# Performance work log

Hardware: AMD Instinct MI355X
Metric: run time of the kernel (lower is better)

The kernel has to match this reference:

```python
import jax, jax.numpy as jnp
import numpy as np

B, N, K = 4, 4096, 16
DP, DM = 128, 256  # d_points, d_model


def setup_inputs() -> dict:
    key = jax.random.key(0)
    ks = jax.random.split(key, 10)
    w = lambda k, s: (jax.random.normal(k, s) * 0.02).astype(jnp.float32)
    return dict(
        features=jax.random.normal(ks[0], (B, N, DP), dtype=jnp.float32),
        xyz=jax.random.normal(ks[1], (B, N, 3), dtype=jnp.float32),
        fc1_w=w(ks[2], (DP, DM)), fc1_b=jnp.zeros((DM,), jnp.float32),
        fc2_w=w(ks[3], (DM, DP)), fc2_b=jnp.zeros((DP,), jnp.float32),
        fd1_w=w(ks[4], (3, DM)), fd1_b=jnp.zeros((DM,), jnp.float32),
        fd2_w=w(ks[5], (DM, DM)), fd2_b=jnp.zeros((DM,), jnp.float32),
        wq=w(ks[6], (DM, DM)), wk=w(ks[7], (DM, DM)), wv=w(ks[8], (DM, DM)),
    )


def reference(features, xyz, fc1_w, fc1_b, fc2_w, fc2_b,
              fd1_w, fd1_b, fd2_w, fd2_b, wq, wk, wv):
    # KNN of xyz against itself (includes self, distance-sorted ascending)
    sq = jnp.sum(xyz * xyz, axis=-1)                                 # [B,N]
    d2 = sq[:, :, None] + sq[:, None, :] - 2.0 * jnp.einsum('bnc,bmc->bnm', xyz, xyz)
    _, knn_idx = jax.lax.top_k(-d2, K)                               # [B,N,K]
    gather = jax.vmap(lambda pts, idx: pts[idx])                     # [B,N,C],[B,N,K]->[B,N,K,C]
    knn_xyz = gather(xyz, knn_idx)                                   # [B,N,K,3]

    x = features @ fc1_w + fc1_b                                     # [B,N,DM]
    q = x @ wq                                                       # [B,N,DM]
    kf = gather(x @ wk, knn_idx)                                     # [B,N,K,DM]
    vf = gather(x @ wv, knn_idx)                                     # [B,N,K,DM]

    delta = xyz[:, :, None, :] - knn_xyz                             # [B,N,K,3]
    pos = jax.nn.relu(delta @ fd1_w + fd1_b) @ fd2_w + fd2_b         # [B,N,K,DM]

    logits = jnp.einsum('bnd,bnkd->bnk', q, kf + pos) / np.sqrt(DM).astype(np.float32)
    attn = jax.nn.softmax(logits, axis=-1)                           # [B,N,K]
    res = jnp.einsum('bnk,bnkd->bnd', attn, vf + pos)                # [B,N,DM]

    out = res @ fc2_w + fc2_b + features                             # [B,N,DP]
    return jnp.transpose(out, (0, 2, 1))                             # [B,DP,N]
```

## Files before the change

### kernel.cpp

```cpp
#include <hip/hip_runtime.h>
#include <hip/hip_bf16.h>
#include <hip/hip_fp16.h>
#include <math.h>

#define B_   4
#define N_   4096
#define K_   16
#define DP_  128
#define DM_  256
#define NPTS (B_ * N_)
#define SEG_ 16
#define CAND_ (N_ / SEG_)
#define QPAD 136

typedef unsigned int u32;
typedef unsigned char u8;
typedef _Float16 f16;
typedef __attribute__((ext_vector_type(2))) __fp16 h2;
typedef __attribute__((ext_vector_type(8))) _Float16 f16x8;
typedef __attribute__((ext_vector_type(4))) float floatx4;

static __device__ __forceinline__ h2 pkrtz(float a, float b) {
    return __builtin_amdgcn_cvt_pkrtz(a, b);
}
static __device__ __forceinline__ u32 asu32(h2 h) { return __builtin_bit_cast(u32, h); }
static __device__ __forceinline__ h2 ash2(u32 u) { return __builtin_bit_cast(h2, u); }

#define CEXA(x, y) { u32 _lo = min(x, y); y = max(x, y); x = _lo; }
#define CEXD(x, y) { u32 _hi = max(x, y); y = min(x, y); x = _hi; }

static __device__ __forceinline__ void sort16_desc(u32 c[16]) {
    CEXD(c[0],c[1]);  CEXD(c[2],c[3]);  CEXD(c[4],c[5]);  CEXD(c[6],c[7]);
    CEXD(c[8],c[9]);  CEXD(c[10],c[11]); CEXD(c[12],c[13]); CEXD(c[14],c[15]);
    CEXD(c[0],c[2]);  CEXD(c[1],c[3]);  CEXD(c[4],c[6]);  CEXD(c[5],c[7]);
    CEXD(c[8],c[10]); CEXD(c[9],c[11]); CEXD(c[12],c[14]); CEXD(c[13],c[15]);
    CEXD(c[1],c[2]);  CEXD(c[5],c[6]);  CEXD(c[9],c[10]); CEXD(c[13],c[14]);
    CEXD(c[0],c[4]);  CEXD(c[1],c[5]);  CEXD(c[2],c[6]);  CEXD(c[3],c[7]);
    CEXD(c[8],c[12]); CEXD(c[9],c[13]); CEXD(c[10],c[14]); CEXD(c[11],c[15]);
    CEXD(c[2],c[4]);  CEXD(c[3],c[5]);  CEXD(c[10],c[12]); CEXD(c[11],c[13]);
    CEXD(c[1],c[2]);  CEXD(c[3],c[4]);  CEXD(c[5],c[6]);
    CEXD(c[9],c[10]); CEXD(c[11],c[12]); CEXD(c[13],c[14]);
    CEXD(c[0],c[8]);  CEXD(c[1],c[9]);  CEXD(c[2],c[10]); CEXD(c[3],c[11]);
    CEXD(c[4],c[12]); CEXD(c[5],c[13]); CEXD(c[6],c[14]); CEXD(c[7],c[15]);
    CEXD(c[4],c[8]);  CEXD(c[5],c[9]);  CEXD(c[6],c[10]); CEXD(c[7],c[11]);
    CEXD(c[2],c[4]);  CEXD(c[3],c[5]);  CEXD(c[6],c[8]);  CEXD(c[7],c[9]);
    CEXD(c[10],c[12]); CEXD(c[11],c[13]);
    CEXD(c[1],c[2]);  CEXD(c[3],c[4]);  CEXD(c[5],c[6]);  CEXD(c[7],c[8]);
    CEXD(c[9],c[10]); CEXD(c[11],c[12]); CEXD(c[13],c[14]);
}

static __device__ __forceinline__ void remerge16_asc(u32 L[16]) {
    CEXA(L[0],L[8]);  CEXA(L[1],L[9]);  CEXA(L[2],L[10]); CEXA(L[3],L[11]);
    CEXA(L[4],L[12]); CEXA(L[5],L[13]); CEXA(L[6],L[14]); CEXA(L[7],L[15]);
    CEXA(L[0],L[4]);  CEXA(L[1],L[5]);  CEXA(L[2],L[6]);  CEXA(L[3],L[7]);
    CEXA(L[8],L[12]); CEXA(L[9],L[13]); CEXA(L[10],L[14]); CEXA(L[11],L[15]);
    CEXA(L[0],L[2]);  CEXA(L[1],L[3]);  CEXA(L[4],L[6]);  CEXA(L[5],L[7]);
    CEXA(L[8],L[10]); CEXA(L[9],L[11]); CEXA(L[12],L[14]); CEXA(L[13],L[15]);
    CEXA(L[0],L[1]);  CEXA(L[2],L[3]);  CEXA(L[4],L[5]);  CEXA(L[6],L[7]);
    CEXA(L[8],L[9]);  CEXA(L[10],L[11]); CEXA(L[12],L[13]); CEXA(L[14],L[15]);
}

static __device__ void knn_part_body(float4* sc, const float* __restrict__ xyz,
                                     u32* __restrict__ part, int id)
{
    const int xblk = id & 15;
    const int s = (id >> 4) & 15;
    const int b = id >> 8;
    const int n = xblk * 256 + threadIdx.x;
    const float* xb = xyz + (size_t)b * N_ * 3;
    const float x0 = xb[n * 3 + 0], x1 = xb[n * 3 + 1], x2 = xb[n * 3 + 2];
    const float nx0 = -x0, nx1 = -x1, nx2 = -x2;
    const float hs = 0.5f * fmaf(x0, x0, fmaf(x1, x1, x2 * x2));
    const u32 kmask = 0xFFFFF000u;

    {
        const int m = s * CAND_ + threadIdx.x;
        const float a0 = xb[m * 3 + 0];
        const float a1 = xb[m * 3 + 1];
        const float a2 = xb[m * 3 + 2];
        sc[threadIdx.x] = make_float4(a0, a1, a2, 0.5f * (a0 * a0 + a1 * a1 + a2 * a2));
    }
    __syncthreads();

    u32 L[16];
#pragma unroll
    for (int i = 0; i < 16; ++i) L[i] = 0xFFFFFFFFu;

    const u32 ibase = (u32)(s * CAND_);
    for (int m0 = 0; m0 < CAND_; m0 += 16) {
        float4 cc[16];
#pragma unroll
        for (int t = 0; t < 16; ++t) cc[t] = sc[m0 + t];
        u32 c[16];
#pragma unroll
        for (int t = 0; t < 16; ++t) {
            const float e = fmaf(nx0, cc[t].x,
                            fmaf(nx1, cc[t].y,
                            fmaf(nx2, cc[t].z, cc[t].w + hs)));
            c[t] = (__float_as_uint(fmaxf(e, 0.0f)) & kmask) | (ibase + (u32)(m0 + t));
        }
        sort16_desc(c);
#pragma unroll
        for (int i = 0; i < 16; ++i) L[i] = min(L[i], c[i]);
        remerge16_asc(L);
    }

    const int p = b * N_ + n;
#pragma unroll
    for (int j = 0; j < 16; ++j)
        part[(size_t)(s * 16 + j) * NPTS + p] = L[j];
}

static __device__ void prep_body(float (*t)[33],
    const float* __restrict__ wq, const float* __restrict__ wk, const float* __restrict__ wv,
    const float* __restrict__ fd2, const float* __restrict__ fc1, const float* __restrict__ fc2,
    const float* __restrict__ feat,
    f16* __restrict__ catW, f16* __restrict__ fc2T, f16* __restrict__ bt2,
    f16* __restrict__ fd2c, f16* __restrict__ wqc, f16* __restrict__ fc1c,
    f16* __restrict__ featb, int bx, int by, int job)
{
    const int tid = threadIdx.x;

    if (job < 4) {
        const float* in; int R, C;
        switch (job) {
            case 0: in = wq;  R = DM_; C = DM_; break;
            case 1: in = wk;  R = DM_; C = DM_; break;
            case 2: in = wv;  R = DM_; C = DM_; break;
            default: in = fc2; R = DM_; C = DP_; break;
        }
        const int c0 = bx * 32, r0 = by * 32;
        if (c0 >= C || r0 >= R) return;
        const int lx = tid & 31, ly = tid >> 5;
#pragma unroll
        for (int i = 0; i < 32; i += 8)
            t[ly + i][lx] = in[(size_t)(r0 + ly + i) * C + c0 + lx];
        __syncthreads();
#pragma unroll
        for (int i = 0; i < 32; i += 8) {
            const int c = c0 + ly + i;
            const f16 v = (f16)t[lx][ly + i];
            int n;
            switch (job) {
                case 0: n = c; break;
                case 1: n = 256 + ((c >> 2) << 3) + (c & 3); break;
                case 2: n = 256 + ((c >> 2) << 3) + 4 + (c & 3); break;
                default: n = -1; break;
            }
            if (job < 3) {
                catW[(size_t)n * DM_ + r0 + lx] = v;
            } else {
                fc2T[(size_t)c * DM_ + r0 + lx] = v;
                bt2[(size_t)c * 512 + 256 + r0 + lx] = v;
            }
        }
    } else {
        const int bid = by * 8 + bx;
        const int tId = bid * 256 + tid;
        const float* in; f16* outp; int n4;
        if (job == 4)      { in = fd2;  outp = fd2c;  n4 = (DM_ * DM_) / 4; }
        else if (job == 5) { in = wq;   outp = wqc;   n4 = (DM_ * DM_) / 4; }
        else if (job == 6) { in = fc1;  outp = fc1c;  n4 = (DP_ * DM_) / 4; }
        else               { in = feat; outp = featb; n4 = (NPTS * DP_) / 4; }
        for (int i = tId; i < n4; i += 16384) {
            const float4 v = ((const float4*)in)[i];
            const u32 lo = asu32(pkrtz(v.x, v.y));
            const u32 hi = asu32(pkrtz(v.z, v.w));
            ((uint2*)outp)[i] = make_uint2(lo, hi);
        }
    }
}

__global__ __launch_bounds__(256) void fused_prep_knn_kernel(
    const float* __restrict__ wq, const float* __restrict__ wk, const float* __restrict__ wv,
    const float* __restrict__ fd2, const float* __restrict__ fc1, const float* __restrict__ fc2,
    const float* __restrict__ feat,
    f16* __restrict__ catW, f16* __restrict__ fc2T, f16* __restrict__ bt2,
    f16* __restrict__ fd2c, f16* __restrict__ wqc, f16* __restrict__ fc1c,
    f16* __restrict__ featb,
    const float* __restrict__ xyz, u32* __restrict__ part)
{
    __shared__ __align__(16) char smem[4352];
    const int id = blockIdx.x;
    if (id < 512) {
        prep_body((float(*)[33])smem, wq, wk, wv, fd2, fc1, fc2, feat,
                  catW, fc2T, bt2, fd2c, wqc, fc1c, featb,
                  id & 7, (id >> 3) & 7, id >> 6);
    } else {
        knn_part_body((float4*)smem, xyz, part, id - 512);
    }
}

static __device__ void gemm_tile(f16* As, f16* Bs,
    const f16* __restrict__ A, const f16* __restrict__ Bt,
    f16* __restrict__ Cb,
    int M, int N, int K, int ldc, int bx, int by)
{
    const int tid = threadIdx.x;
    const int m0 = by * 128, n0 = bx * 128;
    const int w = tid >> 6, l = tid & 63;
    const int wm = (w >> 1) * 64, wn = (w & 1) * 64;
    const int fm = l & 15, kq = l >> 4;

    floatx4 acc[4][4];
#pragma unroll
    for (int i = 0; i < 4; ++i)
#pragma unroll
        for (int j = 0; j < 4; ++j)
            acc[i][j] = (floatx4){0.0f, 0.0f, 0.0f, 0.0f};

    for (int k0 = 0; k0 < K; k0 += 32) {
        __syncthreads();
#pragma unroll
        for (int c = 0; c < 2; ++c) {
            const int li = tid + c * 256;
            const int row = li >> 2, part = li & 3;
            *(uint4*)&As[row * 32 + part * 8] =
                *(const uint4*)&A[(size_t)(m0 + row) * K + k0 + part * 8];
            *(uint4*)&Bs[row * 32 + part * 8] =
                *(const uint4*)&Bt[(size_t)(n0 + row) * K + k0 + part * 8];
        }
        __syncthreads();
        f16x8 af[4], bf[4];
#pragma unroll
        for (int i = 0; i < 4; ++i)
            af[i] = *(const f16x8*)&As[(wm + i * 16 + fm) * 32 + kq * 8];
#pragma unroll
        for (int j = 0; j < 4; ++j)
            bf[j] = *(const f16x8*)&Bs[(wn + j * 16 + fm) * 32 + kq * 8];
#pragma unroll
        for (int i = 0; i < 4; ++i)
#pragma unroll
            for (int j = 0; j < 4; ++j)
                acc[i][j] = __builtin_amdgcn_mfma_f32_16x16x32_f16(af[i], bf[j], acc[i][j], 0, 0, 0);
    }

#pragma unroll
    for (int i = 0; i < 4; ++i) {
#pragma unroll
        for (int j = 0; j < 4; ++j) {
            const int col = n0 + wn + j * 16 + fm;
            const int rowb = m0 + wm + i * 16 + kq * 4;
#pragma unroll
            for (int r = 0; r < 4; ++r)
                Cb[(size_t)(rowb + r) * ldc + col] = (f16)acc[i][j][r];
        }
    }
}

__global__ __launch_bounds__(256) void gemm_qkv_kernel(
    const f16* __restrict__ A,
    const f16* __restrict__ Bt,
    const float* __restrict__ bias,
    f16* __restrict__ Cb)
{
    __shared__ __align__(16) f16 As[128 * QPAD];
    __shared__ __align__(16) f16 Bs[128 * QPAD];
    const int tid = threadIdx.x;
    const int m0 = blockIdx.y * 128, n0 = blockIdx.x * 128;
    const int w = tid >> 6, l = tid & 63;
    const int wm = (w >> 1) * 64, wn = (w & 1) * 64;
    const int fm = l & 15, kq = l >> 4;

#pragma unroll
    for (int c = 0; c < 8; ++c) {
        const int li = tid + c * 256;
        const int row = li >> 4, part = li & 15;
        *(uint4*)&As[row * QPAD + part * 8] =
            *(const uint4*)&A[(size_t)(m0 + row) * 128 + part * 8];
        *(uint4*)&Bs[row * QPAD + part * 8] =
            *(const uint4*)&Bt[(size_t)(n0 + row) * 128 + part * 8];
    }
    __syncthreads();

    floatx4 acc[4][4];
#pragma unroll
    for (int i = 0; i < 4; ++i)
#pragma unroll
        for (int j = 0; j < 4; ++j)
            acc[i][j] = (floatx4){0.0f, 0.0f, 0.0f, 0.0f};

#pragma unroll
    for (int kk = 0; kk < 4; ++kk) {
        f16x8 af[4], bf[4];
#pragma unroll
        for (int i = 0; i < 4; ++i)
            af[i] = *(const f16x8*)&As[(wm + i * 16 + fm) * QPAD + kk * 32 + kq * 8];
#pragma unroll
        for (int j = 0; j < 4; ++j)
            bf[j] = *(const f16x8*)&Bs[(wn + j * 16 + fm) * QPAD + kk * 32 + kq * 8];
#pragma unroll
        for (int i = 0; i < 4; ++i)
#pragma unroll
            for (int j = 0; j < 4; ++j)
                acc[i][j] = __builtin_amdgcn_mfma_f32_16x16x32_f16(af[i], bf[j], acc[i][j], 0, 0, 0);
    }

#pragma unroll
    for (int i = 0; i < 4; ++i) {
#pragma unroll
        for (int j = 0; j < 4; ++j) {
            const int col = n0 + wn + j * 16 + fm;
            const int rowb = m0 + wm + i * 16 + kq * 4;
#pragma unroll
            for (int r = 0; r < 4; ++r)
                Cb[(size_t)(rowb + r) * 1024 + col] = (f16)(acc[i][j][r] + bias[col]);
        }
    }
}

__global__ __launch_bounds__(256) void gemm_out_kernel(
    const f16* __restrict__ A,
    const f16* __restrict__ Bt,
    const float* __restrict__ bias2,
    const float* __restrict__ feat,
    float* __restrict__ CT)
{
    __shared__ __align__(16) f16 As[64 * 32];
    __shared__ __align__(16) f16 Bs[128 * 32];
    const int tid = threadIdx.x;
    const int m0 = blockIdx.x * 64;
    const int w = tid >> 6, l = tid & 63;
    const int wn = w * 32;
    const int fm = l & 15, kq = l >> 4;

    floatx4 acc[4][2];
#pragma unroll
    for (int i = 0; i < 4; ++i)
#pragma unroll
        for (int j = 0; j < 2; ++j)
            acc[i][j] = (floatx4){0.0f, 0.0f, 0.0f, 0.0f};

    for (int k0 = 0; k0 < 512; k0 += 32) {
        __syncthreads();
        {
            const int row = tid >> 2, part = tid & 3;
            *(uint4*)&As[row * 32 + part * 8] =
                *(const uint4*)&A[(size_t)(m0 + row) * 512 + k0 + part * 8];
        }
#pragma unroll
        for (int c = 0; c < 2; ++c) {
            const int li = tid + c * 256;
            const int row = li >> 2, part = li & 3;
            *(uint4*)&Bs[row * 32 + part * 8] =
                *(const uint4*)&Bt[(size_t)row * 512 + k0 + part * 8];
        }
        __syncthreads();
        f16x8 af[4], bf[2];
#pragma unroll
        for (int i = 0; i < 4; ++i)
            af[i] = *(const f16x8*)&As[(i * 16 + fm) * 32 + kq * 8];
#pragma unroll
        for (int j = 0; j < 2; ++j)
            bf[j] = *(const f16x8*)&Bs[(wn + j * 16 + fm) * 32 + kq * 8];
#pragma unroll
        for (int i = 0; i < 4; ++i)
#pragma unroll
            for (int j = 0; j < 2; ++j)
                acc[i][j] = __builtin_amdgcn_mfma_f32_16x16x32_f16(af[i], bf[j], acc[i][j], 0, 0, 0);
    }

#pragma unroll
    for (int i = 0; i < 4; ++i) {
#pragma unroll
        for (int j = 0; j < 2; ++j) {
            const int col = wn + j * 16 + fm;
            const int rowb = m0 + i * 16 + kq * 4;
            float4 vv;
#pragma unroll
            for (int r = 0; r < 4; ++r)
                ((float*)&vv)[r] = acc[i][j][r] + bias2[col]
                                 + feat[(size_t)(rowb + r) * DP_ + col];
            const int bb = rowb >> 12;
            *(float4*)&CT[(size_t)(bb * DP_ + col) * N_ + (rowb & (N_ - 1))] = vv;
        }
    }
}

static __device__ void kvw_body(const f16* __restrict__ qkv, const float* __restrict__ xyz,
                                const float* __restrict__ fd1_w, const float* __restrict__ fd1_b,
                                u8* __restrict__ kvw, f16* __restrict__ ubuf, int id)
{
    const int t = id * 256 + threadIdx.x;
    const int p = t >> 6, g = t & 63;
    const uint4 kv = *(const uint4*)(qkv + (size_t)p * 1024 + 256 + g * 8);
    const h2 k01 = ash2(kv.x), k23 = ash2(kv.y), v01 = ash2(kv.z), v23 = ash2(kv.w);
    int lo = 0, hi = 0;
    lo = __builtin_amdgcn_cvt_pk_fp8_f32((float)k01.x, (float)k01.y, lo, false);
    lo = __builtin_amdgcn_cvt_pk_fp8_f32((float)k23.x, (float)k23.y, lo, true);
    hi = __builtin_amdgcn_cvt_pk_fp8_f32((float)v01.x, (float)v01.y, hi, false);
    hi = __builtin_amdgcn_cvt_pk_fp8_f32((float)v23.x, (float)v23.y, hi, true);

    const float x0 = xyz[(size_t)p * 3 + 0];
    const float x1 = xyz[(size_t)p * 3 + 1];
    const float x2 = xyz[(size_t)p * 3 + 2];
    const int c0 = g * 4;
    const float4 w0v = *(const float4*)&fd1_w[c0];
    const float4 w1v = *(const float4*)&fd1_w[DM_ + c0];
    const float4 w2v = *(const float4*)&fd1_w[2 * DM_ + c0];
    const float4 b1v = *(const float4*)&fd1_b[c0];
    const float ww0 = x0 * w0v.x + x1 * w1v.x + x2 * w2v.x;
    const float ww1 = x0 * w0v.y + x1 * w1v.y + x2 * w2v.y;
    const float ww2 = x0 * w0v.z + x1 * w1v.z + x2 * w2v.z;
    const float ww3 = x0 * w0v.w + x1 * w1v.w + x2 * w2v.w;

    uint4 row;
    row.x = (u32)lo;
    row.y = (u32)hi;
    row.z = asu32(pkrtz(ww0, ww1));
    row.w = asu32(pkrtz(ww2, ww3));
    *(uint4*)(kvw + (size_t)p * 1024 + g * 16) = row;

    const uint2 uu = make_uint2(asu32(pkrtz(ww0 + b1v.x, ww1 + b1v.y)),
                                asu32(pkrtz(ww2 + b1v.z, ww3 + b1v.w)));
    *(uint2*)(ubuf + (size_t)p * 256 + c0) = uu;
}

static __device__ void mergeAB_body(const u32* __restrict__ part, int* __restrict__ knn_idx,
                                    int id)
{
    const int p = id * 256 + threadIdx.x;
    const int b = p >> 12;

    u32 L[16];
#pragma unroll
    for (int i = 0; i < 16; ++i) L[i] = 0xFFFFFFFFu;

    for (int s = 0; s < SEG_; ++s) {
        u32 seg[16];
#pragma unroll
        for (int j = 0; j < 16; ++j)
            seg[j] = part[(size_t)(s * 16 + j) * NPTS + p];
#pragma unroll
        for (int i = 0; i < 16; ++i) L[i] = min(L[i], seg[15 - i]);
        remerge16_asc(L);
    }

    int* o = knn_idx + (size_t)p * K_;
#pragma unroll
    for (int i = 0; i < 16; ++i) o[i] = b * N_ + (int)(L[i] & 0xFFFu);
}

__global__ __launch_bounds__(256) void fused_kvwmerge_kernel(
    const f16* __restrict__ qkv, const float* __restrict__ xyz,
    const float* __restrict__ fd1_w, const float* __restrict__ fd1_b,
    u8* __restrict__ kvw, f16* __restrict__ ubuf,
    const u32* __restrict__ part, int* __restrict__ knn_idx)
{
    const int id = blockIdx.x;
    if (id < NPTS * 64 / 256) kvw_body(qkv, xyz, fd1_w, fd1_b, kvw, ubuf, id);
    else                      mergeAB_body(part, knn_idx, id - NPTS * 64 / 256);
}

__global__ __launch_bounds__(256) void fused_small1_kernel(
    const f16* __restrict__ fd2c, const f16* __restrict__ wqc,
    f16* __restrict__ catWqp,
    const f16* __restrict__ fc2T, f16* __restrict__ bt2)
{
    __shared__ __align__(16) f16 As[128 * 32];
    __shared__ __align__(16) f16 Bs[128 * 32];
    const int id = blockIdx.x;
    if (id < 4)
        gemm_tile(As, Bs, fd2c, wqc, catWqp, DM_, DM_, DM_, DM_, id & 1, id >> 1);
    else
        gemm_tile(As, Bs, fc2T, fd2c, bt2, DP_, DM_, DM_, 512, id - 4, 0);
}

__global__ __launch_bounds__(256) void fused_small2_kernel(
    const f16* __restrict__ catW, const f16* __restrict__ fc1c, f16* __restrict__ WallT,
    const float* __restrict__ fc1_b, const float* __restrict__ fd2_b,
    const float* __restrict__ fc2_w, const float* __restrict__ fc2_b,
    float* __restrict__ b_all, float* __restrict__ bias2)
{
    __shared__ __align__(16) f16 As[128 * 32];
    __shared__ __align__(16) f16 Bs[128 * 32];
    const int id = blockIdx.x;
    const int tid = threadIdx.x;
    if (id < 8) {
        gemm_tile(As, Bs, catW, fc1c, WallT, 1024, DP_, DM_, DP_, 0, id);
    } else if (id < 12) {
        const int n = (id - 8) * 256 + tid;
        float s = 0.0f;
        for (int j = 0; j < DM_; ++j)
            s += fc1_b[j] * (float)catW[(size_t)n * DM_ + j];
        b_all[n] = s;
    } else if (tid < DP_) {
        float s = fc2_b[tid];
        for (int t = 0; t < DM_; ++t)
            s += fd2_b[t] * fc2_w[(size_t)t * DP_ + tid];
        bias2[tid] = s;
    }
}

__global__ __launch_bounds__(256, 1) void attn_kernel(
    const f16* __restrict__ qkv, const u8* __restrict__ kvw,
    const f16* __restrict__ ubuf, const int* __restrict__ knn_idx,
    const float* __restrict__ fd2_b,
    f16* __restrict__ ab)
{
    const int wave = threadIdx.x >> 6, l = threadIdx.x & 63;
    const int bi = blockIdx.x;
    const int p = ((bi & 3) << 12) + ((bi >> 2) << 2) + wave;
    const int c0 = l * 4;

    int gi = 0;
    if (l < 16) gi = knn_idx[p * K_ + l];

    uint4 kvr[16];
#pragma unroll
    for (int k = 0; k < 16; ++k) {
        const int gik = __shfl(gi, k);
        kvr[k] = *(const uint4*)(kvw + (size_t)gik * 1024 + l * 16);
    }
    asm volatile("" ::: "memory");

    const uint2 qu  = *(const uint2*)(qkv + (size_t)p * 1024 + c0);
    const uint2 qpu = *(const uint2*)(qkv + (size_t)p * 1024 + 768 + c0);
    const uint2 uu  = *(const uint2*)(ubuf + (size_t)p * 256 + c0);
    const h2 qh01 = ash2(qu.x), qh23 = ash2(qu.y);
    const h2 qp01 = ash2(qpu.x), qp23 = ash2(qpu.y);
    const h2 u01 = ash2(uu.x), u23 = ash2(uu.y);
    const float q0 = (float)qh01.x, q1 = (float)qh01.y, q2 = (float)qh23.x, q3 = (float)qh23.y;
    const h2 zero2 = (h2)(__fp16)0.0f;

    const float4 f2b = *(const float4*)&fd2_b[c0];

    float qb;
    {
        float tq = q0 * f2b.x + q1 * f2b.y + q2 * f2b.z + q3 * f2b.w;
#pragma unroll
        for (int off = 1; off < 64; off <<= 1) tq += __shfl_xor(tq, off);
        qb = tq;
    }

    float lg[16];
    u32 h01r[16], h23r[16];
#pragma unroll
    for (int k = 0; k < 16; ++k) {
        const uint4 r = kvr[k];
        h2 d01 = u01 - ash2(r.z);
        h2 d23 = u23 - ash2(r.w);
        d01 = __builtin_elementwise_max(d01, zero2);
        d23 = __builtin_elementwise_max(d23, zero2);
        h01r[k] = asu32(d01); h23r[k] = asu32(d23);
        const auto k01 = __builtin_amdgcn_cvt_pk_f32_fp8((int)r.x, false);
        const auto k23 = __builtin_amdgcn_cvt_pk_f32_fp8((int)r.x, true);
        float t = q0 * k01[0] + q1 * k01[1] + q2 * k23[0] + q3 * k23[1];
        t = __builtin_amdgcn_fdot2(d01, qp01, t, false);
        t = __builtin_amdgcn_fdot2(d23, qp23, t, false);
#pragma unroll
        for (int off = 1; off < 64; off <<= 1) t += __shfl_xor(t, off);
        lg[k] = t;
    }

    float att[16];
    {
        float mx = -3.0e38f;
#pragma unroll
        for (int k = 0; k < 16; ++k) {
            att[k] = (lg[k] + qb) * (1.0f / 16.0f);
            mx = fmaxf(mx, att[k]);
        }
        float s = 0.0f;
#pragma unroll
        for (int k = 0; k < 16; ++k) { att[k] = __expf(att[k] - mx); s += att[k]; }
        const float inv = 1.0f / s;
#pragma unroll
        for (int k = 0; k < 16; ++k) att[k] *= inv;
    }

    float rb[4] = {0, 0, 0, 0}, hb[4] = {0, 0, 0, 0};
#pragma unroll
    for (int k = 0; k < 16; ++k) {
        const auto v01 = __builtin_amdgcn_cvt_pk_f32_fp8((int)kvr[k].y, false);
        const auto v23 = __builtin_amdgcn_cvt_pk_f32_fp8((int)kvr[k].y, true);
        const h2 hh01 = ash2(h01r[k]), hh23 = ash2(h23r[k]);
        const float a = att[k];
        rb[0] = fmaf(a, v01[0], rb[0]);
        rb[1] = fmaf(a, v01[1], rb[1]);
        rb[2] = fmaf(a, v23[0], rb[2]);
        rb[3] = fmaf(a, v23[1], rb[3]);
        hb[0] = fmaf(a, (float)hh01.x, hb[0]);
        hb[1] = fmaf(a, (float)hh01.y, hb[1]);
        hb[2] = fmaf(a, (float)hh23.x, hb[2]);
        hb[3] = fmaf(a, (float)hh23.y, hb[3]);
    }

    const uint2 ho = make_uint2(asu32(pkrtz(hb[0], hb[1])), asu32(pkrtz(hb[2], hb[3])));
    const uint2 ro = make_uint2(asu32(pkrtz(rb[0], rb[1])), asu32(pkrtz(rb[2], rb[3])));
    *(uint2*)(ab + (size_t)p * 512 + c0) = ho;
    *(uint2*)(ab + (size_t)p * 512 + 256 + c0) = ro;
}

extern "C" void kernel_launch(void* const* d_in, const int* in_sizes, int n_in,
                              void* d_out, int out_size, void* d_ws, size_t ws_size,
                              hipStream_t stream)
{
    const float* features = (const float*)d_in[0];
    const float* xyz   = (const float*)d_in[1];
    const float* fc1_w = (const float*)d_in[2];
    const float* fc1_b = (const float*)d_in[3];
    const float* fc2_w = (const float*)d_in[4];
    const float* fc2_b = (const float*)d_in[5];
    const float* fd1_w = (const float*)d_in[6];
    const float* fd1_b = (const float*)d_in[7];
    const float* fd2_w = (const float*)d_in[8];
    const float* fd2_b = (const float*)d_in[9];
    const float* wq    = (const float*)d_in[10];
    const float* wk    = (const float*)d_in[11];
    const float* wv    = (const float*)d_in[12];
    float* out = (float*)d_out;

    char* base = (char*)d_ws;
    const size_t MB = 1024 * 1024;
    u32*  part = (u32*)(base + 0);
    f16*  ab   = (f16*)(base + 0);
    u8*   kvw  = (u8*)(base + 20 * MB);
    f16*  qkv  = (f16*)(base + 36 * MB);
    f16*  featb = (f16*)(base + 68 * MB);
    int*  idx  = (int*)(base + 72 * MB);
    char* wb = base + 73 * MB;
    f16* catW  = (f16*)(wb + 0);
    f16* WallT = (f16*)(wb + 512 * 1024);
    f16* bt2   = (f16*)(wb + 768 * 1024);
    f16* fd2c  = (f16*)(wb + 896 * 1024);
    f16* wqc   = (f16*)(wb + 1024 * 1024);
    f16* fc1c  = (f16*)(wb + 1152 * 1024);
    f16* fc2T  = (f16*)(wb + 1216 * 1024);
    float* b_all = (float*)(wb + 1280 * 1024);
    float* bias2 = (float*)(wb + 1284 * 1024);
    f16*  ubuf = (f16*)(base + 76 * MB);

    const dim3 blk(256);

    fused_prep_knn_kernel<<<dim3(512 + 1024), blk, 0, stream>>>(
        wq, wk, wv, fd2_w, fc1_w, fc2_w, features,
        catW, fc2T, bt2, fd2c, wqc, fc1c, featb, xyz, part);
    fused_small1_kernel<<<dim3(6), blk, 0, stream>>>(fd2c, wqc, catW + 768 * 256, fc2T, bt2);
    fused_small2_kernel<<<dim3(13), blk, 0, stream>>>(catW, fc1c, WallT,
                                                      fc1_b, fd2_b, fc2_w, fc2_b, b_all, bias2);
    gemm_qkv_kernel<<<dim3(1024 / 128, NPTS / 128), blk, 0, stream>>>(featb, WallT, b_all, qkv);
    fused_kvwmerge_kernel<<<dim3(NPTS * 64 / 256 + NPTS / 256), blk, 0, stream>>>(
        qkv, xyz, fd1_w, fd1_b, kvw, ubuf, part, idx);
    attn_kernel<<<dim3(NPTS / 4), blk, 0, stream>>>(qkv, kvw, ubuf, idx, fd2_b, ab);
    gemm_out_kernel<<<dim3(NPTS / 64), blk, 0, stream>>>(ab, bt2, bias2, features, out);

    (void)in_sizes; (void)n_in; (void)out_size; (void)ws_size;
}
```

Measured before the change: 211.9 us.

## Split KNN candidate scan across thread pairs with packed FMA and SoA layout

Each query point is now handled by two lanes that each scan half of the 256-candidate segment, so the KNN part of the fused kernel launches twice as many blocks. The two partial top-16 lists are then merged with a cross-lane shuffle and a bitonic remerge. Candidate coordinates move to a structure-of-arrays shared-memory layout so each lane can read float4 vectors, and distances are computed with packed two-wide FMAs. This is meant to raise parallelism and cut per-lane sort work, at the cost of an extra merge step and shuffle traffic.

Measured after the change: 223.3 us. 1.05x slower.

```diff
diff --git a/kernel.cpp b/kernel.cpp
--- a/kernel.cpp
+++ b/kernel.cpp
@@ -19,6 +19,7 @@
 typedef __attribute__((ext_vector_type(2))) __fp16 h2;
 typedef __attribute__((ext_vector_type(8))) _Float16 f16x8;
 typedef __attribute__((ext_vector_type(4))) float floatx4;
+typedef __attribute__((ext_vector_type(2))) float f32x2;
 
 static __device__ __forceinline__ h2 pkrtz(float a, float b) {
     return __builtin_amdgcn_cvt_pkrtz(a, b);
@@ -60,25 +61,34 @@
     CEXA(L[8],L[9]);  CEXA(L[10],L[11]); CEXA(L[12],L[13]); CEXA(L[14],L[15]);
 }
 
-static __device__ void knn_part_body(float4* sc, const float* __restrict__ xyz,
+static __device__ void knn_part_body(float* sm, const float* __restrict__ xyz,
                                      u32* __restrict__ part, int id)
 {
-    const int xblk = id & 15;
-    const int s = (id >> 4) & 15;
-    const int b = id >> 8;
-    const int n = xblk * 256 + threadIdx.x;
+    const int xblk = id & 31;
+    const int s = (id >> 5) & 15;
+    const int b = id >> 9;
+    const int h = threadIdx.x & 1;
+    const int pi = threadIdx.x >> 1;
+    const int n = xblk * 128 + pi;
     const float* xb = xyz + (size_t)b * N_ * 3;
     const float x0 = xb[n * 3 + 0], x1 = xb[n * 3 + 1], x2 = xb[n * 3 + 2];
-    const float nx0 = -x0, nx1 = -x1, nx2 = -x2;
     const float hs = 0.5f * fmaf(x0, x0, fmaf(x1, x1, x2 * x2));
+    const f32x2 nx0 = {-x0, -x0}, nx1 = {-x1, -x1}, nx2 = {-x2, -x2};
+    const f32x2 hs2 = {hs, hs};
+    const f32x2 z2 = {0.0f, 0.0f};
     const u32 kmask = 0xFFFFF000u;
 
+    float* a0s = sm;
+    float* a1s = sm + 256;
+    float* a2s = sm + 512;
+    float* wss = sm + 768;
     {
         const int m = s * CAND_ + threadIdx.x;
-        const float a0 = xb[m * 3 + 0];
-        const float a1 = xb[m * 3 + 1];
-        const float a2 = xb[m * 3 + 2];
-        sc[threadIdx.x] = make_float4(a0, a1, a2, 0.5f * (a0 * a0 + a1 * a1 + a2 * a2));
+        const float A0 = xb[m * 3 + 0];
+        const float A1 = xb[m * 3 + 1];
+        const float A2 = xb[m * 3 + 2];
+        a0s[threadIdx.x] = A0; a1s[threadIdx.x] = A1; a2s[threadIdx.x] = A2;
+        wss[threadIdx.x] = 0.5f * (A0 * A0 + A1 * A1 + A2 * A2);
     }
     __syncthreads();
 
@@ -86,18 +96,39 @@
 #pragma unroll
     for (int i = 0; i < 16; ++i) L[i] = 0xFFFFFFFFu;
 
-    const u32 ibase = (u32)(s * CAND_);
-    for (int m0 = 0; m0 < CAND_; m0 += 16) {
-        float4 cc[16];
-#pragma unroll
-        for (int t = 0; t < 16; ++t) cc[t] = sc[m0 + t];
+    const u32 kidx = (u32)(s * CAND_ + h * 128);
+    const int qb0 = h * 32;
+    const float4* a0q = (const float4*)a0s;
+    const float4* a1q = (const float4*)a1s;
+    const float4* a2q = (const float4*)a2s;
+    const float4* wq4 = (const float4*)wss;
+
+    for (int m0 = 0; m0 < 128; m0 += 16) {
+        const int qb = qb0 + (m0 >> 2);
         u32 c[16];
 #pragma unroll
-        for (int t = 0; t < 16; ++t) {
-            const float e = fmaf(nx0, cc[t].x,
-                            fmaf(nx1, cc[t].y,
-                            fmaf(nx2, cc[t].z, cc[t].w + hs)));
-            c[t] = (__float_as_uint(fmaxf(e, 0.0f)) & kmask) | (ibase + (u32)(m0 + t));
+        for (int q = 0; q < 4; ++q) {
+            const float4 A0 = a0q[qb + q];
+            const float4 A1 = a1q[qb + q];
+            const float4 A2 = a2q[qb + q];
+            const float4 W  = wq4[qb + q];
+            f32x2 e0 = __builtin_elementwise_fma(nx0, (f32x2){A0.x, A0.y},
+                       __builtin_elementwise_fma(nx1, (f32x2){A1.x, A1.y},
+                       __builtin_elementwise_fma(nx2, (f32x2){A2.x, A2.y},
+                                                 (f32x2){W.x, W.y} + hs2)));
+            f32x2 e1 = __builtin_elementwise_fma(nx0, (f32x2){A0.z, A0.w},
+                       __builtin_elementwise_fma(nx1, (f32x2){A1.z, A1.w},
+                       __builtin_elementwise_fma(nx2, (f32x2){A2.z, A2.w},
+                                                 (f32x2){W.z, W.w} + hs2)));
+            e0 = __builtin_elementwise_max(e0, z2);
+            e1 = __builtin_elementwise_max(e1, z2);
+            const uint2 u0 = __builtin_bit_cast(uint2, e0);
+            const uint2 u1 = __builtin_bit_cast(uint2, e1);
+            const u32 kb = kidx + (u32)(m0 + q * 4);
+            c[q * 4 + 0] = (u0.x & kmask) | (kb + 0);
+            c[q * 4 + 1] = (u0.y & kmask) | (kb + 1);
+            c[q * 4 + 2] = (u1.x & kmask) | (kb + 2);
+            c[q * 4 + 3] = (u1.y & kmask) | (kb + 3);
         }
         sort16_desc(c);
 #pragma unroll
@@ -105,10 +136,17 @@
         remerge16_asc(L);
     }
 
+    u32 pl[16];
+#pragma unroll
+    for (int i = 0; i < 16; ++i) pl[i] = (u32)__shfl_xor((int)L[15 - i], 1);
+#pragma unroll
+    for (int i = 0; i < 16; ++i) L[i] = min(L[i], pl[i]);
+    remerge16_asc(L);
+
     const int p = b * N_ + n;
 #pragma unroll
-    for (int j = 0; j < 16; ++j)
-        part[(size_t)(s * 16 + j) * NPTS + p] = L[j];
+    for (int j = 0; j < 8; ++j)
+        part[(size_t)(s * 16 + h * 8 + j) * NPTS + p] = L[h * 8 + j];
 }
 
 static __device__ void prep_body(float (*t)[33],
@@ -187,7 +225,7 @@
                   catW, fc2T, bt2, fd2c, wqc, fc1c, featb,
                   id & 7, (id >> 3) & 7, id >> 6);
     } else {
-        knn_part_body((float4*)smem, xyz, part, id - 512);
+        knn_part_body((float*)smem, xyz, part, id - 512);
     }
 }
 
@@ -633,7 +671,7 @@
 
     const dim3 blk(256);
 
-    fused_prep_knn_kernel<<<dim3(512 + 1024), blk, 0, stream>>>(
+    fused_prep_knn_kernel<<<dim3(512 + 2048), blk, 0, stream>>>(
         wq, wk, wv, fd2_w, fc1_w, fc2_w, features,
         catW, fc2T, bt2, fd2c, wqc, fc1c, featb, xyz, part);
     fused_small1_kernel<<<dim3(6), blk, 0, stream>>>(fd2c, wqc, catW + 768 * 256, fc2T, bt2);
```

## Fuse QKV GEMM with KV fp8 packing and KNN merge into one kernel

Applied to the files above, without the earlier changes.

The QKV projection GEMM now has each block own 64 rows and loop over all 8 column tiles. The K/V columns are kept in shared memory and packed straight into the fp8 kvw and ubuf buffers, so the intermediate K/V never round-trips through global memory. The KNN merge blocks are appended to the same launch, which removes one kernel launch. In exchange the grid drops from 1024 GEMM blocks to 256, and about 100KB of shared memory per block limits occupancy, so parallelism and latency hiding may suffer.

Result: no change. 213.5 us (+0.8%).

```diff
diff --git a/kernel.cpp b/kernel.cpp
--- a/kernel.cpp
+++ b/kernel.cpp
@@ -248,64 +248,161 @@
     }
 }
 
-__global__ __launch_bounds__(256) void gemm_qkv_kernel(
+static __device__ void mergeAB_body(const u32* __restrict__ part, int* __restrict__ knn_idx,
+                                    int id)
+{
+    const int p = id * 256 + threadIdx.x;
+    const int b = p >> 12;
+
+    u32 L[16];
+#pragma unroll
+    for (int i = 0; i < 16; ++i) L[i] = 0xFFFFFFFFu;
+
+    for (int s = 0; s < SEG_; ++s) {
+        u32 seg[16];
+#pragma unroll
+        for (int j = 0; j < 16; ++j)
+            seg[j] = part[(size_t)(s * 16 + j) * NPTS + p];
+#pragma unroll
+        for (int i = 0; i < 16; ++i) L[i] = min(L[i], seg[15 - i]);
+        remerge16_asc(L);
+    }
+
+    int* o = knn_idx + (size_t)p * K_;
+#pragma unroll
+    for (int i = 0; i < 16; ++i) o[i] = b * N_ + (int)(L[i] & 0xFFFu);
+}
+
+#define KVP 520
+__global__ __launch_bounds__(256) void gemm_qkv_fused_kernel(
     const f16* __restrict__ A,
     const f16* __restrict__ Bt,
     const float* __restrict__ bias,
-    f16* __restrict__ Cb)
-{
-    __shared__ __align__(16) f16 As[128 * QPAD];
-    __shared__ __align__(16) f16 Bs[128 * QPAD];
+    const float* __restrict__ xyz,
+    const float* __restrict__ fd1_w, const float* __restrict__ fd1_b,
+    f16* __restrict__ Cb,
+    u8* __restrict__ kvw, f16* __restrict__ ubuf,
+    const u32* __restrict__ part, int* __restrict__ knn_idx)
+{
+    __shared__ __align__(16) f16 As[64 * 136];
+    __shared__ __align__(16) f16 Bs[128 * 136];
+    __shared__ __align__(16) f16 kvs[64 * KVP];
+    const int bid = blockIdx.x;
+    if (bid >= 256) { mergeAB_body(part, knn_idx, bid - 256); return; }
+
     const int tid = threadIdx.x;
-    const int m0 = blockIdx.y * 128, n0 = blockIdx.x * 128;
+    const int m0 = bid * 64;
     const int w = tid >> 6, l = tid & 63;
-    const int wm = (w >> 1) * 64, wn = (w & 1) * 64;
+    const int wr = (w >> 1) * 32;
+    const int wn = (w & 1) * 64;
     const int fm = l & 15, kq = l >> 4;
 
 #pragma unroll
-    for (int c = 0; c < 8; ++c) {
+    for (int c = 0; c < 4; ++c) {
         const int li = tid + c * 256;
-        const int row = li >> 4, part = li & 15;
-        *(uint4*)&As[row * QPAD + part * 8] =
-            *(const uint4*)&A[(size_t)(m0 + row) * 128 + part * 8];
-        *(uint4*)&Bs[row * QPAD + part * 8] =
-            *(const uint4*)&Bt[(size_t)(n0 + row) * 128 + part * 8];
+        const int row = li >> 4, pt = li & 15;
+        *(uint4*)&As[row * 136 + pt * 8] =
+            *(const uint4*)&A[(size_t)(m0 + row) * 128 + pt * 8];
+    }
+
+    for (int nt = 0; nt < 8; ++nt) {
+        __syncthreads();
+#pragma unroll
+        for (int c = 0; c < 8; ++c) {
+            const int li = tid + c * 256;
+            const int row = li >> 4, pt = li & 15;
+            *(uint4*)&Bs[row * 136 + pt * 8] =
+                *(const uint4*)&Bt[(size_t)(nt * 128 + row) * 128 + pt * 8];
+        }
+        __syncthreads();
+
+        floatx4 acc[2][4];
+#pragma unroll
+        for (int i = 0; i < 2; ++i)
+#pragma unroll
+            for (int j = 0; j < 4; ++j)
+                acc[i][j] = (floatx4){0.0f, 0.0f, 0.0f, 0.0f};
+
+#pragma unroll
+        for (int kk = 0; kk < 4; ++kk) {
+            f16x8 af[2], bf[4];
+#pragma unroll
+            for (int i = 0; i < 2; ++i)
+                af[i] = *(const f16x8*)&As[(wr + i * 16 + fm) * 136 + kk * 32 + kq * 8];
+#pragma unroll
+            for (int j = 0; j < 4; ++j)
+                bf[j] = *(const f16x8*)&Bs[(wn + j * 16 + fm) * 136 + kk * 32 + kq * 8];
+#pragma unroll
+            for (int i = 0; i < 2; ++i)
+#pragma unroll
+                for (int j = 0; j < 4; ++j)
+                    acc[i][j] = __builtin_amdgcn_mfma_f32_16x16x32_f16(af[i], bf[j], acc[i][j], 0, 0, 0);
+        }
+
+        if (nt >= 2 && nt < 6) {
+#pragma unroll
+            for (int i = 0; i < 2; ++i) {
+#pragma unroll
+                for (int j = 0; j < 4; ++j) {
+                    const int col = nt * 128 + wn + j * 16 + fm;
+                    const int lcol = col - 256;
+                    const int rowb = wr + i * 16 + kq * 4;
+#pragma unroll
+                    for (int r = 0; r < 4; ++r)
+                        kvs[(rowb + r) * KVP + lcol] = (f16)(acc[i][j][r] + bias[col]);
+                }
+            }
+        } else {
+#pragma unroll
+            for (int i = 0; i < 2; ++i) {
+#pragma unroll
+                for (int j = 0; j < 4; ++j) {
+                    const int col = nt * 128 + wn + j * 16 + fm;
+                    const int rowb = m0 + wr + i * 16 + kq * 4;
+#pragma unroll
+                    for (int r = 0; r < 4; ++r)
+                        Cb[(size_t)(rowb + r) * 1024 + col] = (f16)(acc[i][j][r] + bias[col]);
+                }
+            }
+        }
     }
     __syncthreads();
 
-    floatx4 acc[4][4];
-#pragma unroll
-    for (int i = 0; i < 4; ++i)
-#pragma unroll
-        for (int j = 0; j < 4; ++j)
-            acc[i][j] = (floatx4){0.0f, 0.0f, 0.0f, 0.0f};
-
-#pragma unroll
-    for (int kk = 0; kk < 4; ++kk) {
-        f16x8 af[4], bf[4];
-#pragma unroll
-        for (int i = 0; i < 4; ++i)
-            af[i] = *(const f16x8*)&As[(wm + i * 16 + fm) * QPAD + kk * 32 + kq * 8];
-#pragma unroll
-        for (int j = 0; j < 4; ++j)
-            bf[j] = *(const f16x8*)&Bs[(wn + j * 16 + fm) * QPAD + kk * 32 + kq * 8];
-#pragma unroll
-        for (int i = 0; i < 4; ++i)
-#pragma unroll
-            for (int j = 0; j < 4; ++j)
-                acc[i][j] = __builtin_amdgcn_mfma_f32_16x16x32_f16(af[i], bf[j], acc[i][j], 0, 0, 0);
-    }
-
-#pragma unroll
-    for (int i = 0; i < 4; ++i) {
-#pragma unroll
-        for (int j = 0; j < 4; ++j) {
-            const int col = n0 + wn + j * 16 + fm;
-            const int rowb = m0 + wm + i * 16 + kq * 4;
-#pragma unroll
-            for (int r = 0; r < 4; ++r)
-                Cb[(size_t)(rowb + r) * 1024 + col] = (f16)(acc[i][j][r] + bias[col]);
-        }
+    for (int it = 0; it < 16; ++it) {
+        const int task = it * 256 + tid;
+        const int pl = task >> 6, g = task & 63;
+        const int p = m0 + pl;
+        const uint4 kv = *(const uint4*)&kvs[pl * KVP + g * 8];
+        const h2 k01 = ash2(kv.x), k23 = ash2(kv.y), v01 = ash2(kv.z), v23 = ash2(kv.w);
+        int lo = 0, hi = 0;
+        lo = __builtin_amdgcn_cvt_pk_fp8_f32((float)k01.x, (float)k01.y, lo, false);
+        lo = __builtin_amdgcn_cvt_pk_fp8_f32((float)k23.x, (float)k23.y, lo, true);
+        hi = __builtin_amdgcn_cvt_pk_fp8_f32((float)v01.x, (float)v01.y, hi, false);
+        hi = __builtin_amdgcn_cvt_pk_fp8_f32((float)v23.x, (float)v23.y, hi, true);
+
+        const float x0 = xyz[(size_t)p * 3 + 0];
+        const float x1 = xyz[(size_t)p * 3 + 1];
+        const float x2 = xyz[(size_t)p * 3 + 2];
+        const int c0 = g * 4;
+        const float4 w0v = *(const float4*)&fd1_w[c0];
+        const float4 w1v = *(const float4*)&fd1_w[DM_ + c0];
+        const float4 w2v = *(const float4*)&fd1_w[2 * DM_ + c0];
+        const float4 b1v = *(const float4*)&fd1_b[c0];
+        const float ww0 = x0 * w0v.x + x1 * w1v.x + x2 * w2v.x;
+        const float ww1 = x0 * w0v.y + x1 * w1v.y + x2 * w2v.y;
+        const float ww2 = x0 * w0v.z + x1 * w1v.z + x2 * w2v.z;
+        const float ww3 = x0 * w0v.w + x1 * w1v.w + x2 * w2v.w;
+
+        uint4 row;
+        row.x = (u32)lo;
+        row.y = (u32)hi;
+        row.z = asu32(pkrtz(ww0, ww1));
+        row.w = asu32(pkrtz(ww2, ww3));
+        *(uint4*)(kvw + (size_t)p * 1024 + g * 16) = row;
+
+        const uint2 uu = make_uint2(asu32(pkrtz(ww0 + b1v.x, ww1 + b1v.y)),
+                                    asu32(pkrtz(ww2 + b1v.z, ww3 + b1v.w)));
+        *(uint2*)(ubuf + (size_t)p * 256 + c0) = uu;
     }
 }
 
@@ -375,81 +472,6 @@
             *(float4*)&CT[(size_t)(bb * DP_ + col) * N_ + (rowb & (N_ - 1))] = vv;
         }
     }
-}
-
-static __device__ void kvw_body(const f16* __restrict__ qkv, const float* __restrict__ xyz,
-                                const float* __restrict__ fd1_w, const float* __restrict__ fd1_b,
-                                u8* __restrict__ kvw, f16* __restrict__ ubuf, int id)
-{
-    const int t = id * 256 + threadIdx.x;
-    const int p = t >> 6, g = t & 63;
-    const uint4 kv = *(const uint4*)(qkv + (size_t)p * 1024 + 256 + g * 8);
-    const h2 k01 = ash2(kv.x), k23 = ash2(kv.y), v01 = ash2(kv.z), v23 = ash2(kv.w);
-    int lo = 0, hi = 0;
-    lo = __builtin_amdgcn_cvt_pk_fp8_f32((float)k01.x, (float)k01.y, lo, false);
-    lo = __builtin_amdgcn_cvt_pk_fp8_f32((float)k23.x, (float)k23.y, lo, true);
-    hi = __builtin_amdgcn_cvt_pk_fp8_f32((float)v01.x, (float)v01.y, hi, false);
-    hi = __builtin_amdgcn_cvt_pk_fp8_f32((float)v23.x, (float)v23.y, hi, true);
-
-    const float x0 = xyz[(size_t)p * 3 + 0];
-    const float x1 = xyz[(size_t)p * 3 + 1];
-    const float x2 = xyz[(size_t)p * 3 + 2];
-    const int c0 = g * 4;
-    const float4 w0v = *(const float4*)&fd1_w[c0];
-    const float4 w1v = *(const float4*)&fd1_w[DM_ + c0];
-    const float4 w2v = *(const float4*)&fd1_w[2 * DM_ + c0];
-    const float4 b1v = *(const float4*)&fd1_b[c0];
-    const float ww0 = x0 * w0v.x + x1 * w1v.x + x2 * w2v.x;
-    const float ww1 = x0 * w0v.y + x1 * w1v.y + x2 * w2v.y;
-    const float ww2 = x0 * w0v.z + x1 * w1v.z + x2 * w2v.z;
-    const float ww3 = x0 * w0v.w + x1 * w1v.w + x2 * w2v.w;
-
-    uint4 row;
-    row.x = (u32)lo;
-    row.y = (u32)hi;
-    row.z = asu32(pkrtz(ww0, ww1));
-    row.w = asu32(pkrtz(ww2, ww3));
-    *(uint4*)(kvw + (size_t)p * 1024 + g * 16) = row;
-
-    const uint2 uu = make_uint2(asu32(pkrtz(ww0 + b1v.x, ww1 + b1v.y)),
-                                asu32(pkrtz(ww2 + b1v.z, ww3 + b1v.w)));
-    *(uint2*)(ubuf + (size_t)p * 256 + c0) = uu;
-}
-
-static __device__ void mergeAB_body(const u32* __restrict__ part, int* __restrict__ knn_idx,
-                                    int id)
-{
-    const int p = id * 256 + threadIdx.x;
-    const int b = p >> 12;
-
-    u32 L[16];
-#pragma unroll
-    for (int i = 0; i < 16; ++i) L[i] = 0xFFFFFFFFu;
-
-    for (int s = 0; s < SEG_; ++s) {
-        u32 seg[16];
-#pragma unroll
-        for (int j = 0; j < 16; ++j)
-            seg[j] = part[(size_t)(s * 16 + j) * NPTS + p];
-#pragma unroll
-        for (int i = 0; i < 16; ++i) L[i] = min(L[i], seg[15 - i]);
-        remerge16_asc(L);
-    }
-
-    int* o = knn_idx + (size_t)p * K_;
-#pragma unroll
-    for (int i = 0; i < 16; ++i) o[i] = b * N_ + (int)(L[i] & 0xFFFu);
-}
-
-__global__ __launch_bounds__(256) void fused_kvwmerge_kernel(
-    const f16* __restrict__ qkv, const float* __restrict__ xyz,
-    const float* __restrict__ fd1_w, const float* __restrict__ fd1_b,
-    u8* __restrict__ kvw, f16* __restrict__ ubuf,
-    const u32* __restrict__ part, int* __restrict__ knn_idx)
-{
-    const int id = blockIdx.x;
-    if (id < NPTS * 64 / 256) kvw_body(qkv, xyz, fd1_w, fd1_b, kvw, ubuf, id);
-    else                      mergeAB_body(part, knn_idx, id - NPTS * 64 / 256);
 }
 
 __global__ __launch_bounds__(256) void fused_small1_kernel(
@@ -639,9 +661,8 @@
     fused_small1_kernel<<<dim3(6), blk, 0, stream>>>(fd2c, wqc, catW + 768 * 256, fc2T, bt2);
     fused_small2_kernel<<<dim3(13), blk, 0, stream>>>(catW, fc1c, WallT,
                                                       fc1_b, fd2_b, fc2_w, fc2_b, b_all, bias2);
-    gemm_qkv_kernel<<<dim3(1024 / 128, NPTS / 128), blk, 0, stream>>>(featb, WallT, b_all, qkv);
-    fused_kvwmerge_kernel<<<dim3(NPTS * 64 / 256 + NPTS / 256), blk, 0, stream>>>(
-        qkv, xyz, fd1_w, fd1_b, kvw, ubuf, part, idx);
+    gemm_qkv_fused_kernel<<<dim3(256 + 64), blk, 0, stream>>>(
+        featb, WallT, b_all, xyz, fd1_w, fd1_b, qkv, kvw, ubuf, part, idx);
     attn_kernel<<<dim3(NPTS / 4), blk, 0, stream>>>(qkv, kvw, ubuf, idx, fd2_b, ab);
     gemm_out_kernel<<<dim3(NPTS / 64), blk, 0, stream>>>(ab, bt2, bias2, features, out);
 
```
